# Kernel optimization log

Hardware: AMD Instinct MI355X
Metric: run time of the kernel (lower is better)

The kernel has to match this reference:

```python
import jax, jax.numpy as jnp
import numpy as np

E = 16          # number of experts
K = 2           # top-k routing
D = 1024        # model dim
F = 512         # expert ffn dim
T = 4096        # tokens
C = 2048


def setup_inputs() -> dict:
    key = jax.random.key(0)
    k1, k2, k3, k4, k5, k6 = jax.random.split(key, 6)
    return {
        "hidden_states": jax.random.normal(k1, (T, D), jnp.float32),
        "topk_indices": jax.random.randint(k2, (T, K), 0, E, jnp.int64),
        "topk_weights": jax.random.uniform(k3, (T, K), jnp.float32),
        "w_gate": jax.random.normal(k4, (E, D, F), jnp.float32) * 0.02,
        "w_up": jax.random.normal(k5, (E, D, F), jnp.float32) * 0.02,
        "w_down": jax.random.normal(k6, (E, F, D), jnp.float32) * 0.02,
    }


def reference(hidden_states, topk_indices, topk_weights, w_gate, w_up, w_down):
    Tn, d = hidden_states.shape
    k = topk_indices.shape[1]
    TK = Tn * k

    # ---- dispatch_tokens: group (token, expert) pairs by expert id ----
    flat_e = topk_indices.reshape(-1)                 # [TK] expert id per slot
    flat_w = topk_weights.reshape(-1)                 # [TK]
    flat_t = jnp.arange(TK) // k                      # [TK] source token id
    order = jnp.argsort(flat_e)                       # sort slots by expert
    se, st, sw = flat_e[order], flat_t[order], flat_w[order]
    counts = jnp.bincount(flat_e, length=E)           # tokens per expert
    starts = jnp.cumsum(counts) - counts              # exclusive prefix sum
    pos = jnp.arange(TK) - starts[se]                 # position within expert bucket
    valid = pos < C
    slot = jnp.where(valid, se * C + pos, E * C)      # overflow -> scratch row

    # gather tokens into padded per-expert buffers [E, C, D]
    buf = jnp.zeros((E * C + 1, d), hidden_states.dtype).at[slot].set(hidden_states[st])
    xe = buf[: E * C].reshape(E, C, d)

    # ---- per-expert gated-SiLU MLP via grouped GEMMs ----
    h = jax.nn.silu(jnp.einsum('ecd,edf->ecf', xe, w_gate)) * jnp.einsum('ecd,edf->ecf', xe, w_up)
    ye = jnp.einsum('ecf,efd->ecd', h, w_down).reshape(E * C, d)

    # ---- weighted scatter-add combine (index_add_) ----
    contrib = ye[jnp.minimum(slot, E * C - 1)] * (sw * valid.astype(sw.dtype))[:, None]
    out = jnp.zeros((Tn, d), topk_weights.dtype).at[st].add(contrib)
    return out.astype(hidden_states.dtype)
```

## Files before the change

### kernel.cpp

```cpp
#include <hip/hip_runtime.h>
#include <hip/hip_bf16.h>

constexpr int E_ = 16, K_ = 2, D_ = 1024, F_ = 512, T_ = 4096;
constexpr int TK_ = T_ * K_;
constexpr int CAP_ = 2048;
constexpr int BM_ = 128;
constexpr int ROWS_MAX = 10240;

constexpr size_t SZ_W   = (size_t)E_ * F_ * D_ * 2;
constexpr size_t OFF_WGT  = 0;
constexpr size_t OFF_WUT  = OFF_WGT + SZ_W;
constexpr size_t OFF_WDT  = OFF_WUT + SZ_W;
constexpr size_t OFF_XG   = OFF_WDT + SZ_W;
constexpr size_t SZ_XG  = (size_t)ROWS_MAX * D_ * 2;
constexpr size_t OFF_H    = OFF_XG + SZ_XG;
constexpr size_t SZ_H   = (size_t)ROWS_MAX * F_ * 2;
constexpr size_t OFF_META = OFF_H + SZ_H;

typedef __attribute__((ext_vector_type(8))) short short8;
typedef __attribute__((ext_vector_type(4))) float float4v;

__device__ __forceinline__ unsigned short f2bf(float f) {
  union { float f; unsigned int u; } v; v.f = f;
  unsigned int r = (v.u + 0x7fffu + ((v.u >> 16) & 1u)) >> 16;
  return (unsigned short)r;
}

__device__ __forceinline__ void load_lds16(const unsigned short* g, unsigned short* l) {
  __builtin_amdgcn_global_load_lds(
      (const __attribute__((address_space(1))) unsigned int*)g,
      (__attribute__((address_space(3))) unsigned int*)l,
      16, 0, 0);
}

__launch_bounds__(1024)
__global__ void dispatch_k(const int* __restrict__ idx, const float* __restrict__ tw,
                           int* __restrict__ cnt_c, int* __restrict__ off_al,
                           int* __restrict__ row_token, float* __restrict__ row_weight) {
  __shared__ int hist[E_], offs[E_], ctr[E_];
  int tid = threadIdx.x;
  if (tid < E_) hist[tid] = 0;
  __syncthreads();
  for (int i = tid; i < TK_; i += 1024) atomicAdd(&hist[idx[i]], 1);
  __syncthreads();
  if (tid == 0) {
    int run = 0;
    for (int e = 0; e < E_; ++e) {
      int c = hist[e] > CAP_ ? CAP_ : hist[e];
      cnt_c[e] = c; off_al[e] = run; offs[e] = run; ctr[e] = 0;
      run += (c + BM_ - 1) & ~(BM_ - 1);
    }
  }
  __syncthreads();
  for (int r = tid; r < ROWS_MAX; r += 1024) row_token[r] = -1;
  __syncthreads();
  for (int i = tid; i < TK_; i += 1024) {
    int e = idx[i];
    int r = atomicAdd(&ctr[e], 1);
    if (r < CAP_) {
      int row = offs[e] + r;
      row_token[row] = i >> 1;
      row_weight[row] = tw[i];
    }
  }
}

__global__ void gather_k(const float* __restrict__ hidden, const int* __restrict__ row_token,
                         unsigned short* __restrict__ Xg) {
  int r = blockIdx.x;
  int tok = row_token[r];
  int c = threadIdx.x * 4;
  ushort4 o;
  if (tok >= 0) {
    float4 v = *(const float4*)(hidden + (size_t)tok * D_ + c);
    o.x = f2bf(v.x); o.y = f2bf(v.y); o.z = f2bf(v.z); o.w = f2bf(v.w);
  } else {
    o.x = 0; o.y = 0; o.z = 0; o.w = 0;
  }
  *(ushort4*)(Xg + (size_t)r * D_ + c) = o;
}

__global__ void transpose_all_k(const float* __restrict__ wg, const float* __restrict__ wu,
                                const float* __restrict__ wd,
                                unsigned short* __restrict__ WgT, unsigned short* __restrict__ WuT,
                                unsigned short* __restrict__ WdT) {
  __shared__ float tile[32][33];
  int z = blockIdx.y;
  int kind = z >> 4, e = z & 15;
  int R = (kind == 2) ? F_ : D_;
  int C = (kind == 2) ? D_ : F_;
  const float* s = ((kind == 0) ? wg : (kind == 1) ? wu : wd) + (size_t)e * R * C;
  unsigned short* d = ((kind == 0) ? WgT : (kind == 1) ? WuT : WdT) + (size_t)e * R * C;
  int tilesX = C >> 5;
  int t = blockIdx.x;
  int r0 = (t / tilesX) * 32, c0 = (t % tilesX) * 32;
  int tr = threadIdx.x >> 3;
  int tc = (threadIdx.x & 7) * 4;
  float4 v = *(const float4*)(s + (size_t)(r0 + tr) * C + (c0 + tc));
  tile[tr][tc + 0] = v.x; tile[tr][tc + 1] = v.y;
  tile[tr][tc + 2] = v.z; tile[tr][tc + 3] = v.w;
  __syncthreads();
  ushort4 o;
  o.x = f2bf(tile[tc + 0][tr]);
  o.y = f2bf(tile[tc + 1][tr]);
  o.z = f2bf(tile[tc + 2][tr]);
  o.w = f2bf(tile[tc + 3][tr]);
  *(ushort4*)(d + (size_t)(c0 + tr) * R + (r0 + tc)) = o;
}


__launch_bounds__(256)
__global__ void gemm1_k(const unsigned short* __restrict__ Xg,
                        const unsigned short* __restrict__ WgT,
                        const unsigned short* __restrict__ WuT,
                        unsigned short* __restrict__ Hbuf,
                        const int* __restrict__ cnt_c, const int* __restrict__ off_al) {
  int e = blockIdx.z, mt = blockIdx.y, nt = blockIdx.x;
  int cnt = cnt_c[e];
  if (mt * 128 >= cnt) return;
  int rbase = off_al[e] + mt * 128;

  __shared__ unsigned short lA[128 * 64];
  __shared__ unsigned short lBg[64 * 64];
  __shared__ unsigned short lBu[64 * 64];

  int tid = threadIdx.x, wid = tid >> 6, lane = tid & 63;
  int wm = wid >> 1, wn = wid & 1;
  int quad = lane >> 4, l15 = lane & 15;
  int sw = l15 & 7;

  const unsigned short* gA = Xg + (size_t)rbase * D_;
  const unsigned short* gB0 = WgT + ((size_t)e * F_ + nt * 64) * D_;
  const unsigned short* gB1 = WuT + ((size_t)e * F_ + nt * 64) * D_;

  float4v accg[4][2], accu[4][2];
#pragma unroll
  for (int i = 0; i < 4; ++i)
#pragma unroll
    for (int j = 0; j < 2; ++j) {
      accg[i][j] = (float4v){0.f, 0.f, 0.f, 0.f};
      accu[i][j] = (float4v){0.f, 0.f, 0.f, 0.f};
    }

  for (int k0 = 0; k0 < D_; k0 += 64) {
    __syncthreads();
#pragma unroll
    for (int it = 0; it < 4; ++it) {
      int fw = it * 256 + wid * 64;
      int f = fw + lane;
      int row = f >> 3, c8 = (f & 7) ^ (row & 7);
      load_lds16(gA + (size_t)row * D_ + k0 + c8 * 8, &lA[(size_t)fw * 8]);
    }
#pragma unroll
    for (int it = 0; it < 2; ++it) {
      int fw = it * 256 + wid * 64;
      int f = fw + lane;
      int row = f >> 3, c8 = (f & 7) ^ (row & 7);
      size_t go = (size_t)row * D_ + k0 + c8 * 8;
      load_lds16(gB0 + go, &lBg[(size_t)fw * 8]);
      load_lds16(gB1 + go, &lBu[(size_t)fw * 8]);
    }
    __syncthreads();
#pragma unroll
    for (int kc = 0; kc < 2; ++kc) {
      short8 af[4], bg[2], bu[2];
#pragma unroll
      for (int i = 0; i < 4; ++i) {
        int r = wm * 64 + i * 16 + l15;
        af[i] = *(const short8*)&lA[r * 64 + ((kc * 4 + quad) ^ sw) * 8];
      }
#pragma unroll
      for (int j = 0; j < 2; ++j) {
        int n = wn * 32 + j * 16 + l15;
        bg[j] = *(const short8*)&lBg[n * 64 + ((kc * 4 + quad) ^ sw) * 8];
        bu[j] = *(const short8*)&lBu[n * 64 + ((kc * 4 + quad) ^ sw) * 8];
      }
#pragma unroll
      for (int i = 0; i < 4; ++i)
#pragma unroll
        for (int j = 0; j < 2; ++j) {
          accg[i][j] = __builtin_amdgcn_mfma_f32_16x16x32_bf16(af[i], bg[j], accg[i][j], 0, 0, 0);
          accu[i][j] = __builtin_amdgcn_mfma_f32_16x16x32_bf16(af[i], bu[j], accu[i][j], 0, 0, 0);
        }
    }
  }

  int rem = cnt - mt * 128;
#pragma unroll
  for (int i = 0; i < 4; ++i)
#pragma unroll
    for (int j = 0; j < 2; ++j)
#pragma unroll
      for (int r = 0; r < 4; ++r) {
        int row = wm * 64 + i * 16 + quad * 4 + r;
        if (row < rem) {
          float g = accg[i][j][r], u = accu[i][j][r];
          float h = (g / (1.f + __expf(-g))) * u;
          int n = nt * 64 + wn * 32 + j * 16 + l15;
          Hbuf[(size_t)(rbase + row) * F_ + n] = f2bf(h);
        }
      }
}

__launch_bounds__(256)
__global__ void gemm2_k(const unsigned short* __restrict__ Hbuf,
                        const unsigned short* __restrict__ WdT,
                        float* __restrict__ out,
                        const int* __restrict__ cnt_c, const int* __restrict__ off_al,
                        const int* __restrict__ row_token, const float* __restrict__ row_weight) {
  int e = blockIdx.z, mt = blockIdx.y, nt = blockIdx.x;
  int cnt = cnt_c[e];
  if (mt * 128 >= cnt) return;
  int rbase = off_al[e] + mt * 128;

  __shared__ unsigned short lA[128 * 64];
  __shared__ unsigned short lB[128 * 64];

  int tid = threadIdx.x, wid = tid >> 6, lane = tid & 63;
  int wm = wid >> 1, wn = wid & 1;
  int quad = lane >> 4, l15 = lane & 15;
  int sw = l15 & 7;

  const unsigned short* gA = Hbuf + (size_t)rbase * F_;
  const unsigned short* gB = WdT + ((size_t)e * D_ + nt * 128) * F_;

  float4v acc[4][4];
#pragma unroll
  for (int i = 0; i < 4; ++i)
#pragma unroll
    for (int j = 0; j < 4; ++j) acc[i][j] = (float4v){0.f, 0.f, 0.f, 0.f};

  for (int k0 = 0; k0 < F_; k0 += 64) {
    __syncthreads();
#pragma unroll
    for (int it = 0; it < 4; ++it) {
      int fw = it * 256 + wid * 64;
      int f = fw + lane;
      int row = f >> 3, c8 = (f & 7) ^ (row & 7);
      size_t go = (size_t)row * F_ + k0 + c8 * 8;
      load_lds16(gA + go, &lA[(size_t)fw * 8]);
      load_lds16(gB + go, &lB[(size_t)fw * 8]);
    }
    __syncthreads();
#pragma unroll
    for (int kc = 0; kc < 2; ++kc) {
      short8 af[4], bf[4];
#pragma unroll
      for (int i = 0; i < 4; ++i) {
        int r = wm * 64 + i * 16 + l15;
        af[i] = *(const short8*)&lA[r * 64 + ((kc * 4 + quad) ^ sw) * 8];
      }
#pragma unroll
      for (int j = 0; j < 4; ++j) {
        int n = wn * 64 + j * 16 + l15;
        bf[j] = *(const short8*)&lB[n * 64 + ((kc * 4 + quad) ^ sw) * 8];
      }
#pragma unroll
      for (int i = 0; i < 4; ++i)
#pragma unroll
        for (int j = 0; j < 4; ++j)
          acc[i][j] = __builtin_amdgcn_mfma_f32_16x16x32_bf16(af[i], bf[j], acc[i][j], 0, 0, 0);
    }
  }

  int rem = cnt - mt * 128;
#pragma unroll
  for (int i = 0; i < 4; ++i)
#pragma unroll
    for (int r = 0; r < 4; ++r) {
      int row = wm * 64 + i * 16 + quad * 4 + r;
      if (row < rem) {
        int gr = rbase + row;
        int tok = row_token[gr];
        if (tok >= 0) {
          float w = row_weight[gr];
          float* op = out + (size_t)tok * D_;
#pragma unroll
          for (int j = 0; j < 4; ++j) {
            int n = nt * 128 + wn * 64 + j * 16 + l15;
            atomicAdd(op + n, w * acc[i][j][r]);
          }
        }
      }
    }
}

extern "C" void kernel_launch(void* const* d_in, const int* in_sizes, int n_in,
                              void* d_out, int out_size, void* d_ws, size_t ws_size,
                              hipStream_t stream) {
  const float* hidden  = (const float*)d_in[0];
  const int*   topkidx = (const int*)d_in[1];
  const float* topkw   = (const float*)d_in[2];
  const float* w_gate  = (const float*)d_in[3];
  const float* w_up    = (const float*)d_in[4];
  const float* w_down  = (const float*)d_in[5];
  float* out = (float*)d_out;

  char* ws = (char*)d_ws;
  unsigned short* WgT = (unsigned short*)(ws + OFF_WGT);
  unsigned short* WuT = (unsigned short*)(ws + OFF_WUT);
  unsigned short* WdT = (unsigned short*)(ws + OFF_WDT);
  unsigned short* Xg  = (unsigned short*)(ws + OFF_XG);
  unsigned short* Hb  = (unsigned short*)(ws + OFF_H);
  int* meta           = (int*)(ws + OFF_META);
  int* cnt_c    = meta;
  int* off_al   = meta + 16;
  int* row_token = meta + 32;
  float* row_weight = (float*)(meta + 32 + ROWS_MAX);

  hipMemsetAsync(out, 0, (size_t)out_size * sizeof(float), stream);

  dispatch_k<<<1, 1024, 0, stream>>>(topkidx, topkw, cnt_c, off_al, row_token, row_weight);
  transpose_all_k<<<dim3(512, 48), 256, 0, stream>>>(w_gate, w_up, w_down, WgT, WuT, WdT);
  gather_k<<<ROWS_MAX, 256, 0, stream>>>(hidden, row_token, Xg);

  gemm1_k<<<dim3(F_ / 64, CAP_ / 128, E_), 256, 0, stream>>>(Xg, WgT, WuT, Hb, cnt_c, off_al);
  gemm2_k<<<dim3(D_ / 128, CAP_ / 128, E_), 256, 0, stream>>>(Hb, WdT, out, cnt_c, off_al,
                                                              row_token, row_weight);
}
```

Baseline: 269.9 us.

## Parallelize dispatch across blocks and halve GEMM M-tile to 64 rows

Replaces the single-block dispatch kernel with a multi-block histogram, a tiny offsets kernel and a multi-block slot-assignment kernel, using memsets to zero counters and fill row_token. Halves the M tile in both grouped GEMMs from 128 to 64 rows, which doubles the number of workgroups and cuts padding waste per expert. The smaller tile lowers per-block operand reuse and adds extra weight traffic, plus a few extra launches. The BM padding constant stays 128, so the offsets remain consistent.

Measured after the change: 292.5 us. +8.4%, slower.

```diff
diff --git a/kernel.cpp b/kernel.cpp
--- a/kernel.cpp
+++ b/kernel.cpp
@@ -33,35 +33,34 @@
       16, 0, 0);
 }
 
-__launch_bounds__(1024)
-__global__ void dispatch_k(const int* __restrict__ idx, const float* __restrict__ tw,
-                           int* __restrict__ cnt_c, int* __restrict__ off_al,
-                           int* __restrict__ row_token, float* __restrict__ row_weight) {
-  __shared__ int hist[E_], offs[E_], ctr[E_];
-  int tid = threadIdx.x;
-  if (tid < E_) hist[tid] = 0;
-  __syncthreads();
-  for (int i = tid; i < TK_; i += 1024) atomicAdd(&hist[idx[i]], 1);
-  __syncthreads();
-  if (tid == 0) {
+__global__ void hist_k(const int* __restrict__ idx, int* __restrict__ cnt_raw) {
+  int i = blockIdx.x * 256 + threadIdx.x;
+  atomicAdd(&cnt_raw[idx[i]], 1);
+}
+
+__global__ void offsets_k(const int* __restrict__ cnt_raw, int* __restrict__ cnt_c,
+                          int* __restrict__ off_al) {
+  if (threadIdx.x == 0) {
     int run = 0;
     for (int e = 0; e < E_; ++e) {
-      int c = hist[e] > CAP_ ? CAP_ : hist[e];
-      cnt_c[e] = c; off_al[e] = run; offs[e] = run; ctr[e] = 0;
+      int c = cnt_raw[e]; if (c > CAP_) c = CAP_;
+      cnt_c[e] = c;
+      off_al[e] = run;
       run += (c + BM_ - 1) & ~(BM_ - 1);
     }
   }
-  __syncthreads();
-  for (int r = tid; r < ROWS_MAX; r += 1024) row_token[r] = -1;
-  __syncthreads();
-  for (int i = tid; i < TK_; i += 1024) {
-    int e = idx[i];
-    int r = atomicAdd(&ctr[e], 1);
-    if (r < CAP_) {
-      int row = offs[e] + r;
-      row_token[row] = i >> 1;
-      row_weight[row] = tw[i];
-    }
+}
+
+__global__ void assign_k(const int* __restrict__ idx, const float* __restrict__ tw,
+                         int* __restrict__ cnt2, const int* __restrict__ off_al,
+                         int* __restrict__ row_token, float* __restrict__ row_weight) {
+  int i = blockIdx.x * 256 + threadIdx.x;
+  int e = idx[i];
+  int r = atomicAdd(&cnt2[e], 1);
+  if (r < CAP_) {
+    int row = off_al[e] + r;
+    row_token[row] = i >> 1;
+    row_weight[row] = tw[i];
   }
 }
 
@@ -117,10 +116,10 @@
                         const int* __restrict__ cnt_c, const int* __restrict__ off_al) {
   int e = blockIdx.z, mt = blockIdx.y, nt = blockIdx.x;
   int cnt = cnt_c[e];
-  if (mt * 128 >= cnt) return;
-  int rbase = off_al[e] + mt * 128;
-
-  __shared__ unsigned short lA[128 * 64];
+  if (mt * 64 >= cnt) return;
+  int rbase = off_al[e] + mt * 64;
+
+  __shared__ unsigned short lA[64 * 64];
   __shared__ unsigned short lBg[64 * 64];
   __shared__ unsigned short lBu[64 * 64];
 
@@ -133,9 +132,9 @@
   const unsigned short* gB0 = WgT + ((size_t)e * F_ + nt * 64) * D_;
   const unsigned short* gB1 = WuT + ((size_t)e * F_ + nt * 64) * D_;
 
-  float4v accg[4][2], accu[4][2];
-#pragma unroll
-  for (int i = 0; i < 4; ++i)
+  float4v accg[2][2], accu[2][2];
+#pragma unroll
+  for (int i = 0; i < 2; ++i)
 #pragma unroll
     for (int j = 0; j < 2; ++j) {
       accg[i][j] = (float4v){0.f, 0.f, 0.f, 0.f};
@@ -145,28 +144,22 @@
   for (int k0 = 0; k0 < D_; k0 += 64) {
     __syncthreads();
 #pragma unroll
-    for (int it = 0; it < 4; ++it) {
+    for (int it = 0; it < 2; ++it) {
+      int s = it * 256 + wid * 64 + lane;
+      int row = s >> 3, c8 = (s & 7) ^ (row & 7);
+      size_t go = (size_t)row * D_ + k0 + c8 * 8;
       int fw = it * 256 + wid * 64;
-      int f = fw + lane;
-      int row = f >> 3, c8 = (f & 7) ^ (row & 7);
-      load_lds16(gA + (size_t)row * D_ + k0 + c8 * 8, &lA[(size_t)fw * 8]);
-    }
-#pragma unroll
-    for (int it = 0; it < 2; ++it) {
-      int fw = it * 256 + wid * 64;
-      int f = fw + lane;
-      int row = f >> 3, c8 = (f & 7) ^ (row & 7);
-      size_t go = (size_t)row * D_ + k0 + c8 * 8;
+      load_lds16(gA + go, &lA[(size_t)fw * 8]);
       load_lds16(gB0 + go, &lBg[(size_t)fw * 8]);
       load_lds16(gB1 + go, &lBu[(size_t)fw * 8]);
     }
     __syncthreads();
 #pragma unroll
     for (int kc = 0; kc < 2; ++kc) {
-      short8 af[4], bg[2], bu[2];
-#pragma unroll
-      for (int i = 0; i < 4; ++i) {
-        int r = wm * 64 + i * 16 + l15;
+      short8 af[2], bg[2], bu[2];
+#pragma unroll
+      for (int i = 0; i < 2; ++i) {
+        int r = wm * 32 + i * 16 + l15;
         af[i] = *(const short8*)&lA[r * 64 + ((kc * 4 + quad) ^ sw) * 8];
       }
 #pragma unroll
@@ -176,7 +169,7 @@
         bu[j] = *(const short8*)&lBu[n * 64 + ((kc * 4 + quad) ^ sw) * 8];
       }
 #pragma unroll
-      for (int i = 0; i < 4; ++i)
+      for (int i = 0; i < 2; ++i)
 #pragma unroll
         for (int j = 0; j < 2; ++j) {
           accg[i][j] = __builtin_amdgcn_mfma_f32_16x16x32_bf16(af[i], bg[j], accg[i][j], 0, 0, 0);
@@ -185,14 +178,14 @@
     }
   }
 
-  int rem = cnt - mt * 128;
-#pragma unroll
-  for (int i = 0; i < 4; ++i)
+  int rem = cnt - mt * 64;
+#pragma unroll
+  for (int i = 0; i < 2; ++i)
 #pragma unroll
     for (int j = 0; j < 2; ++j)
 #pragma unroll
       for (int r = 0; r < 4; ++r) {
-        int row = wm * 64 + i * 16 + quad * 4 + r;
+        int row = wm * 32 + i * 16 + quad * 4 + r;
         if (row < rem) {
           float g = accg[i][j][r], u = accu[i][j][r];
           float h = (g / (1.f + __expf(-g))) * u;
@@ -210,10 +203,10 @@
                         const int* __restrict__ row_token, const float* __restrict__ row_weight) {
   int e = blockIdx.z, mt = blockIdx.y, nt = blockIdx.x;
   int cnt = cnt_c[e];
-  if (mt * 128 >= cnt) return;
-  int rbase = off_al[e] + mt * 128;
-
-  __shared__ unsigned short lA[128 * 64];
+  if (mt * 64 >= cnt) return;
+  int rbase = off_al[e] + mt * 64;
+
+  __shared__ unsigned short lA[64 * 64];
   __shared__ unsigned short lB[128 * 64];
 
   int tid = threadIdx.x, wid = tid >> 6, lane = tid & 63;
@@ -224,30 +217,33 @@
   const unsigned short* gA = Hbuf + (size_t)rbase * F_;
   const unsigned short* gB = WdT + ((size_t)e * D_ + nt * 128) * F_;
 
-  float4v acc[4][4];
-#pragma unroll
-  for (int i = 0; i < 4; ++i)
+  float4v acc[2][4];
+#pragma unroll
+  for (int i = 0; i < 2; ++i)
 #pragma unroll
     for (int j = 0; j < 4; ++j) acc[i][j] = (float4v){0.f, 0.f, 0.f, 0.f};
 
   for (int k0 = 0; k0 < F_; k0 += 64) {
     __syncthreads();
 #pragma unroll
+    for (int it = 0; it < 2; ++it) {
+      int s = it * 256 + wid * 64 + lane;
+      int row = s >> 3, c8 = (s & 7) ^ (row & 7);
+      load_lds16(gA + (size_t)row * F_ + k0 + c8 * 8, &lA[(size_t)(it * 256 + wid * 64) * 8]);
+    }
+#pragma unroll
     for (int it = 0; it < 4; ++it) {
-      int fw = it * 256 + wid * 64;
-      int f = fw + lane;
-      int row = f >> 3, c8 = (f & 7) ^ (row & 7);
-      size_t go = (size_t)row * F_ + k0 + c8 * 8;
-      load_lds16(gA + go, &lA[(size_t)fw * 8]);
-      load_lds16(gB + go, &lB[(size_t)fw * 8]);
+      int s = it * 256 + wid * 64 + lane;
+      int row = s >> 3, c8 = (s & 7) ^ (row & 7);
+      load_lds16(gB + (size_t)row * F_ + k0 + c8 * 8, &lB[(size_t)(it * 256 + wid * 64) * 8]);
     }
     __syncthreads();
 #pragma unroll
     for (int kc = 0; kc < 2; ++kc) {
-      short8 af[4], bf[4];
-#pragma unroll
-      for (int i = 0; i < 4; ++i) {
-        int r = wm * 64 + i * 16 + l15;
+      short8 af[2], bf[4];
+#pragma unroll
+      for (int i = 0; i < 2; ++i) {
+        int r = wm * 32 + i * 16 + l15;
         af[i] = *(const short8*)&lA[r * 64 + ((kc * 4 + quad) ^ sw) * 8];
       }
 #pragma unroll
@@ -256,19 +252,19 @@
         bf[j] = *(const short8*)&lB[n * 64 + ((kc * 4 + quad) ^ sw) * 8];
       }
 #pragma unroll
-      for (int i = 0; i < 4; ++i)
+      for (int i = 0; i < 2; ++i)
 #pragma unroll
         for (int j = 0; j < 4; ++j)
           acc[i][j] = __builtin_amdgcn_mfma_f32_16x16x32_bf16(af[i], bf[j], acc[i][j], 0, 0, 0);
     }
   }
 
-  int rem = cnt - mt * 128;
-#pragma unroll
-  for (int i = 0; i < 4; ++i)
+  int rem = cnt - mt * 64;
+#pragma unroll
+  for (int i = 0; i < 2; ++i)
 #pragma unroll
     for (int r = 0; r < 4; ++r) {
-      int row = wm * 64 + i * 16 + quad * 4 + r;
+      int row = wm * 32 + i * 16 + quad * 4 + r;
       if (row < rem) {
         int gr = rbase + row;
         int tok = row_token[gr];
@@ -303,18 +299,25 @@
   unsigned short* Xg  = (unsigned short*)(ws + OFF_XG);
   unsigned short* Hb  = (unsigned short*)(ws + OFF_H);
   int* meta           = (int*)(ws + OFF_META);
-  int* cnt_c    = meta;
-  int* off_al   = meta + 16;
-  int* row_token = meta + 32;
-  float* row_weight = (float*)(meta + 32 + ROWS_MAX);
+  int* cnt_raw   = meta;
+  int* cnt2      = meta + 16;
+  int* cnt_c     = meta + 32;
+  int* off_al    = meta + 48;
+  int* row_token = meta + 64;
+  float* row_weight = (float*)(meta + 64 + ROWS_MAX);
 
   hipMemsetAsync(out, 0, (size_t)out_size * sizeof(float), stream);
-
-  dispatch_k<<<1, 1024, 0, stream>>>(topkidx, topkw, cnt_c, off_al, row_token, row_weight);
+  hipMemsetAsync(meta, 0, 64 * sizeof(int), stream);
+  hipMemsetAsync(row_token, 0xFF, (size_t)ROWS_MAX * sizeof(int), stream);
+
+  hist_k<<<TK_ / 256, 256, 0, stream>>>(topkidx, cnt_raw);
+  offsets_k<<<1, 64, 0, stream>>>(cnt_raw, cnt_c, off_al);
+  assign_k<<<TK_ / 256, 256, 0, stream>>>(topkidx, topkw, cnt2, off_al, row_token, row_weight);
+
   transpose_all_k<<<dim3(512, 48), 256, 0, stream>>>(w_gate, w_up, w_down, WgT, WuT, WdT);
   gather_k<<<ROWS_MAX, 256, 0, stream>>>(hidden, row_token, Xg);
 
-  gemm1_k<<<dim3(F_ / 64, CAP_ / 128, E_), 256, 0, stream>>>(Xg, WgT, WuT, Hb, cnt_c, off_al);
-  gemm2_k<<<dim3(D_ / 128, CAP_ / 128, E_), 256, 0, stream>>>(Hb, WdT, out, cnt_c, off_al,
-                                                              row_token, row_weight);
-}
+  gemm1_k<<<dim3(F_ / 64, CAP_ / 64, E_), 256, 0, stream>>>(Xg, WgT, WuT, Hb, cnt_c, off_al);
+  gemm2_k<<<dim3(D_ / 128, CAP_ / 64, E_), 256, 0, stream>>>(Hb, WdT, out, cnt_c, off_al,
+                                                             row_token, row_weight);
+}
```
